# Kernel optimization log

Measured on AMD Instinct MI355X. Metric: run time of the kernel, lower is better.

## Reference

```python
import jax, jax.numpy as jnp
import numpy as np

# Hodgkin-Huxley / synaptic constants (CFG in the original repo)
GNA, GK, GL = 40.0, 35.0, 0.1
ENA, EK, EL = 55.0, -77.0, -65.0
GS, VS = 0.5, 0.0
IAPP = 0.5
VT, KP = -20.0, 3.0
A_D, A_R = 1.0, 0.1
DT = 0.05


def setup_inputs() -> dict:
    key = jax.random.key(0)
    B, N, L = 32, 2000, 128
    z = jax.random.uniform(key, (B, N, L), dtype=jnp.float32)
    return {"z": z}


def _hh_step(carry, z_prev):
    V, m, n, h, y = carry  # each (B, L)
    pow1 = GNA * m ** 3 * h
    pow2 = GK * n ** 4
    G = DT / 2 * (pow1 + pow2 + GL + GS * y)
    E = pow1 * ENA + pow2 * EK + GL * EL + GS * VS * y
    Vn = (V * (1 - G) + DT * (E + IAPP)) / (1 + G)

    aN = 0.02 * (Vn - 25) / (1 - jnp.exp((-Vn + 25) / 9.0))
    aM = 0.182 * (Vn + 35) / (1 - jnp.exp((-Vn - 35) / 9.0))
    aH = 0.25 * jnp.exp((-Vn - 90) / 12.0)
    bN = -0.002 * (Vn - 25) / (1 - jnp.exp((Vn - 25) / 9.0))
    bM = -0.124 * (Vn + 35) / (1 - jnp.exp((Vn + 35) / 9.0))
    bH = 0.25 * jnp.exp((Vn + 34) / 12.0)
    # removable-singularity fixups (exact equality, as in the original)
    at25 = Vn == 25.0
    atm35 = Vn == -35.0
    aN = jnp.where(at25, 0.18, aN)
    bN = jnp.where(at25, 0.08, bN)
    aM = jnp.where(atm35, 1.638, aM)
    bM = jnp.where(atm35, 1.16, bM)

    def cn(a, b, x):  # semi-implicit (Crank-Nicolson) gating update
        s = DT / 2 * (a + b)
        return (a * DT + (1 - s) * x) / (s + 1)

    mn = cn(aM, bM, m)
    nn = cn(aN, bN, n)
    hn = cn(aH, bH, h)
    sy = DT / 2 * (A_D * z_prev + A_R)
    yn = (A_D * z_prev * DT + (1 - sy) * y) / (sy + 1)
    return (Vn, mn, nn, hn, yn), Vn


def reference(z):
    B, N, L = z.shape
    V0 = jnp.full((B, L), -70.0, dtype=z.dtype)
    m0 = jnp.zeros((B, L), dtype=z.dtype)
    n0 = jnp.zeros((B, L), dtype=z.dtype)
    h0 = jnp.ones((B, L), dtype=z.dtype)
    y0 = jnp.zeros((B, L), dtype=z.dtype)
    zs = jnp.moveaxis(z[:, :-1, :], 1, 0)  # (N-1, B, L)
    _, V_seq = jax.lax.scan(_hh_step, (V0, m0, n0, h0, y0), zs)
    V_all = jnp.concatenate([V0[None], V_seq], axis=0)  # (N, B, L)
    V_all = jnp.moveaxis(V_all, 0, 1)  # (B, N, L)
    return jax.nn.sigmoid((V_all - VT) / KP)
```

## Files before the change

kernel.cpp:

```cpp
#include <hip/hip_runtime.h>


#if defined(__HIP_DEVICE_COMPILE__)
#define EXP2 __builtin_amdgcn_exp2f
#else
#define EXP2 exp2f
#endif

__device__ __forceinline__ float rcpf(float x) { return __builtin_amdgcn_rcpf(x); }

template<int CTRL>
__device__ __forceinline__ float qp(float x) {
#if defined(__HIP_DEVICE_COMPILE__)
    return __int_as_float(__builtin_amdgcn_mov_dpp(__float_as_int(x), CTRL, 0xF, 0xF, false));
#else
    return x;
#endif
}
#define QB0(x) qp<0x00>(x)
#define QB1(x) qp<0x55>(x)
#define QB2(x) qp<0xAA>(x)
#define QB3(x) qp<0xFF>(x)
#define QSW(x) qp<0xB1>(x)

struct LaneC {
    float cA, cB;
    float cC, cD;
    float cE;
    float cH, cK, cL, cM;
    float cAe, cAz, cAt;
    float sing, fB, fA;
};

__device__ __forceinline__ float hh_step4(float& V, float& g, float z,
                                          const LaneC& C) {
    float nn = QB0(g), mm = QB1(g), hh2 = QB2(g), yy = QB3(g);
    float m2 = mm * mm, mh = mm * hh2;
    float p1 = m2 * mh;
    float q  = nn * nn, n4 = q * q;
    float gy1 = __builtin_fmaf(0.0125f, yy, 1.0025f);
    float den = p1 + __builtin_fmaf(0.875f, n4, gy1);
    float rd  = rcpf(den);
    float t1  = __builtin_fmaf(110.0f, p1, -0.3f);
    float t2  = __builtin_fmaf(-134.75f, n4, t1);
    float pre = __builtin_fmaf(2.0f, V, t2);
    float num = __builtin_fmaf(-V, den, pre);
    float Vn  = num * rd;
    float e  = EXP2(__builtin_fmaf(C.cA, Vn, C.cB));
    float t  = __builtin_fmaf(C.cC, Vn, C.cD);
    bool fx  = (Vn == C.sing);
    float br = QSW(e);
    float w  = t * __builtin_fmaf(C.cH, e, C.cK);
    float s  = __builtin_fmaf(C.cL, br, __builtin_fmaf(C.cM, z, w));
    float u  = __builtin_fmaf(-C.cE, e, 1.0f);
    float Q  = u + s;
    float be = u - s;
    float al = __builtin_fmaf(C.cAe, e, __builtin_fmaf(C.cAz, z, C.cAt * t));
    float P  = __builtin_fmaf(be, g, al);
    float gN = P * rcpf(Q);
    float gF = __builtin_fmaf(C.fB, g, C.fA);
    g = fx ? gF : gN;
    V = Vn;
    return Vn;
}

__global__ __launch_bounds__(64, 1)
void hh_kernel(const float* __restrict__ z, float* __restrict__ out, int N) {
    const int gid   = blockIdx.x * 64 + threadIdx.x;
    const int lane  = gid & 3;
    const int chain = gid >> 2;
    const int b = chain >> 7;
    const int l = chain & 127;
    const size_t base = (size_t)b * N * 128 + l;
    const float* zp = z + base;
    float* op = out + base;

    LaneC C;
    const float NaNf = __int_as_float(0x7FC00000);
    switch (lane) {
    case 0:
        C = { -0.1602994490f,  4.0074862250f,  0.02f, -0.5f, 1.0f,
              0.0025f, 0.025f, 0.0f, 0.0f,
              0.0f, 0.0f, 0.05f,
              25.0f, 0.98708396f, 0.0089418778f };
        break;
    case 1:
        C = { -0.1602994490f, -5.6104807150f,  0.182f, 6.37f, 1.0f,
              0.0170329670329670f, 0.025f, 0.0f, 0.0f,
              0.0f, 0.0f, 0.05f,
              -35.0f, 0.86924620f, 0.076545632f };
        break;
    case 2:
        C = { -0.1202245839f, -10.8202125510f, 0.0f, 1.0f, 0.0f,
              0.00625f, 0.0f, 0.00625f, 0.0f,
              0.0125f, 0.0f, 0.0f,
              NaNf, 0.0f, 0.0f };
        break;
    default:
        C = {  0.1202245839f,   4.0876358530f, 0.0f, 1.0f, 0.0f,
              0.0f, 0.0025f, 0.0f, 0.025f,
              0.0f, 0.05f, 0.0f,
              NaNf, 0.0f, 0.0f };
        break;
    }

    float V = -70.0f;
    float g = (lane == 2) ? 1.0f : 0.0f;

    op[0] = -70.0f;

    float z0 = (0 <= N-2) ? zp[0]   : 0.0f;
    float z1 = (1 <= N-2) ? zp[128] : 0.0f;
    float z2 = (2 <= N-2) ? zp[256] : 0.0f;
    float z3 = (3 <= N-2) ? zp[384] : 0.0f;
    float z4 = (4 <= N-2) ? zp[512] : 0.0f;
    float z5 = (5 <= N-2) ? zp[640] : 0.0f;
    float z6 = (6 <= N-2) ? zp[768] : 0.0f;
    float z7 = (7 <= N-2) ? zp[896] : 0.0f;
    const float* zpre = zp + 8 * 128;
    float* o = op + 128;
    int t = 1;
    for (; t <= N - 11; t += 4) {
        float q0 = zpre[0];
        float q1 = zpre[128];
        float q2 = zpre[256];
        float q3 = zpre[384];
        zpre += 512;
        float v0 = hh_step4(V, g, z0, C);
        float v1 = hh_step4(V, g, z1, C);
        float v2 = hh_step4(V, g, z2, C);
        float v3 = hh_step4(V, g, z3, C);
        o[0] = v0; o[128] = v1; o[256] = v2; o[384] = v3;
        o += 512;
        z0 = z4; z1 = z5; z2 = z6; z3 = z7;
        z4 = q0; z5 = q1; z6 = q2; z7 = q3;
    }
    for (; t < N; ++t) {
        float v0 = hh_step4(V, g, z0, C);
        *o = v0;
        o += 128;
        z0 = z1; z1 = z2; z2 = z3; z3 = z4; z4 = z5; z5 = z6; z6 = z7;
        z7 = (t + 7 <= N - 1) ? zpre[0] : 0.0f;
        zpre += 128;
    }
}

__global__ __launch_bounds__(256)
void sig_kernel(float4* __restrict__ v, int n4c) {
    int i = blockIdx.x * 256 + threadIdx.x;
    if (i < n4c) {
        float4 x = v[i];
        x.x = rcpf(1.0f + EXP2(__builtin_fmaf(-0.48089834664f, x.x, -9.6179669328f)));
        x.y = rcpf(1.0f + EXP2(__builtin_fmaf(-0.48089834664f, x.y, -9.6179669328f)));
        x.z = rcpf(1.0f + EXP2(__builtin_fmaf(-0.48089834664f, x.z, -9.6179669328f)));
        x.w = rcpf(1.0f + EXP2(__builtin_fmaf(-0.48089834664f, x.w, -9.6179669328f)));
        v[i] = x;
    }
}

extern "C" void kernel_launch(void* const* d_in, const int* in_sizes, int n_in,
                              void* d_out, int out_size, void* d_ws, size_t ws_size,
                              hipStream_t stream) {
    const float* z = (const float*)d_in[0];
    float* out = (float*)d_out;
    const int B = 32, L = 128;
    const int N = in_sizes[0] / (B * L);
    dim3 grid(B * L * 4 / 64), block(64);
    hipLaunchKernelGGL(hh_kernel, grid, block, 0, stream, z, out, N);
    const int n4c = out_size / 4;
    dim3 sgrid((n4c + 255) / 256), sblock(256);
    hipLaunchKernelGGL(sig_kernel, sgrid, sblock, 0, stream, (float4*)out, n4c);
}
```

Before: 217.2 us.

## Represent gating variables as numerator/denominator pairs to remove reciprocal from recurrence

Each gating variable is now kept as a projective pair (p, q) instead of a single value. The gate update multiplies the denominator rather than dividing, and the voltage formula is cross-multiplied so only one reciprocal stays on the serial chain. Exponent bit manipulation renormalizes q into [0.5, 1) each step to prevent overflow, with p scaled to match. This shortens the loop-carried latency, but it adds many multiplies, extra DPP broadcasts and a different rounding behaviour.

```diff
diff --git a/kernel.cpp b/kernel.cpp
--- a/kernel.cpp
+++ b/kernel.cpp
@@ -32,20 +32,31 @@
     float sing, fB, fA;
 };
 
-__device__ __forceinline__ float hh_step4(float& V, float& g, float z,
+__device__ __forceinline__ float hh_step4(float& V, float& p, float& q, float z,
                                           const LaneC& C) {
-    float nn = QB0(g), mm = QB1(g), hh2 = QB2(g), yy = QB3(g);
-    float m2 = mm * mm, mh = mm * hh2;
-    float p1 = m2 * mh;
-    float q  = nn * nn, n4 = q * q;
-    float gy1 = __builtin_fmaf(0.0125f, yy, 1.0025f);
-    float den = p1 + __builtin_fmaf(0.875f, n4, gy1);
-    float rd  = rcpf(den);
-    float t1  = __builtin_fmaf(110.0f, p1, -0.3f);
-    float t2  = __builtin_fmaf(-134.75f, n4, t1);
-    float pre = __builtin_fmaf(2.0f, V, t2);
-    float num = __builtin_fmaf(-V, den, pre);
-    float Vn  = num * rd;
+    float pn = QB0(p), pm = QB1(p), ph = QB2(p), py = QB3(p);
+    float qn = QB0(q), qm = QB1(q), qh = QB2(q), qy = QB3(q);
+    float pm2 = pm * pm,  qm2 = qm * qm;
+    float pmh = pm * ph,  qmh = qm * qh;
+    float A = pm2 * pmh,  B = qm2 * qmh;
+    float pn2 = pn * pn,  qn2 = qn * qn;
+    float Cc = pn2 * pn2, Dq = qn2 * qn2;
+    float DQy = Dq * qy;
+    float BQy = B * qy;
+    float BDq = B * Dq;
+    float W   = BDq * qy;
+    float AD  = A * DQy;
+    float CB  = Cc * BQy;
+    float PyB = py * BDq;
+    float denW = __builtin_fmaf(0.0125f, PyB,
+                 __builtin_fmaf(0.875f, CB,
+                 __builtin_fmaf(1.0025f, W, AD)));
+    float rdW  = rcpf(denW);
+    float preW = __builtin_fmaf(2.0f, V, -0.3f) * W;
+    float numW = __builtin_fmaf(-V, denW,
+                 __builtin_fmaf(110.0f, AD,
+                 __builtin_fmaf(-134.75f, CB, preW)));
+    float Vn   = numW * rdW;
     float e  = EXP2(__builtin_fmaf(C.cA, Vn, C.cB));
     float t  = __builtin_fmaf(C.cC, Vn, C.cD);
     bool fx  = (Vn == C.sing);
@@ -56,10 +67,16 @@
     float Q  = u + s;
     float be = u - s;
     float al = __builtin_fmaf(C.cAe, e, __builtin_fmaf(C.cAz, z, C.cAt * t));
-    float P  = __builtin_fmaf(be, g, al);
-    float gN = P * rcpf(Q);
-    float gF = __builtin_fmaf(C.fB, g, C.fA);
-    g = fx ? gF : gN;
+    Q  = fx ? 1.0f : Q;
+    be = fx ? C.fB : be;
+    al = fx ? C.fA : al;
+    float pnew = __builtin_fmaf(be, p, al * q);
+    float qnew = Q * q;
+    int qb = __float_as_int(qnew);
+    int ef = (qb >> 23) & 0xFF;
+    q = __int_as_float((qb & 0x807FFFFF) | 0x3F000000);
+    float sc = __int_as_float((253 - ef) << 23);
+    p = pnew * sc;
     V = Vn;
     return Vn;
 }
@@ -105,7 +122,8 @@
     }
 
     float V = -70.0f;
-    float g = (lane == 2) ? 1.0f : 0.0f;
+    float p = (lane == 2) ? 1.0f : 0.0f;
+    float q = 1.0f;
 
     op[0] = -70.0f;
 
@@ -121,22 +139,22 @@
     float* o = op + 128;
     int t = 1;
     for (; t <= N - 11; t += 4) {
-        float q0 = zpre[0];
-        float q1 = zpre[128];
-        float q2 = zpre[256];
-        float q3 = zpre[384];
+        float a0 = zpre[0];
+        float a1 = zpre[128];
+        float a2 = zpre[256];
+        float a3 = zpre[384];
         zpre += 512;
-        float v0 = hh_step4(V, g, z0, C);
-        float v1 = hh_step4(V, g, z1, C);
-        float v2 = hh_step4(V, g, z2, C);
-        float v3 = hh_step4(V, g, z3, C);
+        float v0 = hh_step4(V, p, q, z0, C);
+        float v1 = hh_step4(V, p, q, z1, C);
+        float v2 = hh_step4(V, p, q, z2, C);
+        float v3 = hh_step4(V, p, q, z3, C);
         o[0] = v0; o[128] = v1; o[256] = v2; o[384] = v3;
         o += 512;
         z0 = z4; z1 = z5; z2 = z6; z3 = z7;
-        z4 = q0; z5 = q1; z6 = q2; z7 = q3;
+        z4 = a0; z5 = a1; z6 = a2; z7 = a3;
     }
     for (; t < N; ++t) {
-        float v0 = hh_step4(V, g, z0, C);
+        float v0 = hh_step4(V, p, q, z0, C);
         *o = v0;
         o += 128;
         z0 = z1; z1 = z2; z2 = z3; z3 = z4; z4 = z5; z5 = z6; z6 = z7;
```

Measured after the change: 260.8 us. 20.1% more time.

## Interleave two independent HH chains per thread and halve the grid

Applied to the files above, without the earlier changes.

Each thread now advances two independent neuron chains, (b,l) and (b,l)+2048, with their steps interleaved. The grid shrinks to half as many single-wave blocks. The goal is to hide the long serial dependency latency of each Hodgkin-Huxley step with instruction-level parallelism across chains. The cost is more registers per thread and only half as many CUs in use, so the serial critical path per wave may simply get longer.

```diff
diff --git a/kernel.cpp b/kernel.cpp
--- a/kernel.cpp
+++ b/kernel.cpp
@@ -68,12 +68,15 @@
 void hh_kernel(const float* __restrict__ z, float* __restrict__ out, int N) {
     const int gid   = blockIdx.x * 64 + threadIdx.x;
     const int lane  = gid & 3;
-    const int chain = gid >> 2;
-    const int b = chain >> 7;
-    const int l = chain & 127;
-    const size_t base = (size_t)b * N * 128 + l;
-    const float* zp = z + base;
-    float* op = out + base;
+    const int quad  = gid >> 2;
+    const int bA = quad >> 7,          lA = quad & 127;
+    const int bB = (quad + 2048) >> 7, lB = (quad + 2048) & 127;
+    const size_t baseA = (size_t)bA * N * 128 + lA;
+    const size_t baseB = (size_t)bB * N * 128 + lB;
+    const float* zpA = z + baseA;
+    const float* zpB = z + baseB;
+    float* opA = out + baseA;
+    float* opB = out + baseB;
 
     LaneC C;
     const float NaNf = __int_as_float(0x7FC00000);
@@ -104,44 +107,59 @@
         break;
     }
 
-    float V = -70.0f;
-    float g = (lane == 2) ? 1.0f : 0.0f;
+    float VA = -70.0f, VB = -70.0f;
+    float gA = (lane == 2) ? 1.0f : 0.0f;
+    float gB = gA;
 
-    op[0] = -70.0f;
+    opA[0] = -70.0f;
+    opB[0] = -70.0f;
 
-    float z0 = (0 <= N-2) ? zp[0]   : 0.0f;
-    float z1 = (1 <= N-2) ? zp[128] : 0.0f;
-    float z2 = (2 <= N-2) ? zp[256] : 0.0f;
-    float z3 = (3 <= N-2) ? zp[384] : 0.0f;
-    float z4 = (4 <= N-2) ? zp[512] : 0.0f;
-    float z5 = (5 <= N-2) ? zp[640] : 0.0f;
-    float z6 = (6 <= N-2) ? zp[768] : 0.0f;
-    float z7 = (7 <= N-2) ? zp[896] : 0.0f;
-    const float* zpre = zp + 8 * 128;
-    float* o = op + 128;
+    float a0 = (0 <= N-2) ? zpA[0]   : 0.0f,  b0 = (0 <= N-2) ? zpB[0]   : 0.0f;
+    float a1 = (1 <= N-2) ? zpA[128] : 0.0f,  b1 = (1 <= N-2) ? zpB[128] : 0.0f;
+    float a2 = (2 <= N-2) ? zpA[256] : 0.0f,  b2 = (2 <= N-2) ? zpB[256] : 0.0f;
+    float a3 = (3 <= N-2) ? zpA[384] : 0.0f,  b3 = (3 <= N-2) ? zpB[384] : 0.0f;
+    float a4 = (4 <= N-2) ? zpA[512] : 0.0f,  b4 = (4 <= N-2) ? zpB[512] : 0.0f;
+    float a5 = (5 <= N-2) ? zpA[640] : 0.0f,  b5 = (5 <= N-2) ? zpB[640] : 0.0f;
+    float a6 = (6 <= N-2) ? zpA[768] : 0.0f,  b6 = (6 <= N-2) ? zpB[768] : 0.0f;
+    float a7 = (7 <= N-2) ? zpA[896] : 0.0f,  b7 = (7 <= N-2) ? zpB[896] : 0.0f;
+    const float* zpreA = zpA + 8 * 128;
+    const float* zpreB = zpB + 8 * 128;
+    float* oA = opA + 128;
+    float* oB = opB + 128;
     int t = 1;
     for (; t <= N - 11; t += 4) {
-        float q0 = zpre[0];
-        float q1 = zpre[128];
-        float q2 = zpre[256];
-        float q3 = zpre[384];
-        zpre += 512;
-        float v0 = hh_step4(V, g, z0, C);
-        float v1 = hh_step4(V, g, z1, C);
-        float v2 = hh_step4(V, g, z2, C);
-        float v3 = hh_step4(V, g, z3, C);
-        o[0] = v0; o[128] = v1; o[256] = v2; o[384] = v3;
-        o += 512;
-        z0 = z4; z1 = z5; z2 = z6; z3 = z7;
-        z4 = q0; z5 = q1; z6 = q2; z7 = q3;
+        float qa0 = zpreA[0],   qb0 = zpreB[0];
+        float qa1 = zpreA[128], qb1 = zpreB[128];
+        float qa2 = zpreA[256], qb2 = zpreB[256];
+        float qa3 = zpreA[384], qb3 = zpreB[384];
+        zpreA += 512; zpreB += 512;
+        float vA0 = hh_step4(VA, gA, a0, C);
+        float vB0 = hh_step4(VB, gB, b0, C);
+        float vA1 = hh_step4(VA, gA, a1, C);
+        float vB1 = hh_step4(VB, gB, b1, C);
+        float vA2 = hh_step4(VA, gA, a2, C);
+        float vB2 = hh_step4(VB, gB, b2, C);
+        float vA3 = hh_step4(VA, gA, a3, C);
+        float vB3 = hh_step4(VB, gB, b3, C);
+        oA[0] = vA0; oA[128] = vA1; oA[256] = vA2; oA[384] = vA3;
+        oB[0] = vB0; oB[128] = vB1; oB[256] = vB2; oB[384] = vB3;
+        oA += 512; oB += 512;
+        a0 = a4; a1 = a5; a2 = a6; a3 = a7;
+        a4 = qa0; a5 = qa1; a6 = qa2; a7 = qa3;
+        b0 = b4; b1 = b5; b2 = b6; b3 = b7;
+        b4 = qb0; b5 = qb1; b6 = qb2; b7 = qb3;
     }
     for (; t < N; ++t) {
-        float v0 = hh_step4(V, g, z0, C);
-        *o = v0;
-        o += 128;
-        z0 = z1; z1 = z2; z2 = z3; z3 = z4; z4 = z5; z5 = z6; z6 = z7;
-        z7 = (t + 7 <= N - 1) ? zpre[0] : 0.0f;
-        zpre += 128;
+        float vA0 = hh_step4(VA, gA, a0, C);
+        float vB0 = hh_step4(VB, gB, b0, C);
+        *oA = vA0; *oB = vB0;
+        oA += 128; oB += 128;
+        a0 = a1; a1 = a2; a2 = a3; a3 = a4; a4 = a5; a5 = a6; a6 = a7;
+        b0 = b1; b1 = b2; b2 = b3; b3 = b4; b4 = b5; b5 = b6; b6 = b7;
+        bool ok = (t + 7 <= N - 1);
+        a7 = ok ? zpreA[0] : 0.0f;
+        b7 = ok ? zpreB[0] : 0.0f;
+        zpreA += 128; zpreB += 128;
     }
 }
 
@@ -165,7 +183,7 @@
     float* out = (float*)d_out;
     const int B = 32, L = 128;
     const int N = in_sizes[0] / (B * L);
-    dim3 grid(B * L * 4 / 64), block(64);
+    dim3 grid(B * L * 4 / (2 * 64)), block(64);
     hipLaunchKernelGGL(hh_kernel, grid, block, 0, stream, z, out, N);
     const int n4c = out_size / 4;
     dim3 sgrid((n4c + 255) / 256), sblock(256);
```

Result: slower. 327.0 us (+50.6%).
